# Kernel optimization log

Measured on AMD Instinct MI355X. Metric: run time of the kernel, lower is better.

Reference implementation:

```python
import jax, jax.numpy as jnp
from jax import lax
import numpy as np

NUM_SUBCNNS = 3      # num_classes - 1
C_FEAT = 1024        # backbone feature channels (hard-coded in CAM loop)
STRIDE = 32          # 224 -> 7 spatial reduction, like densenet121 features


def setup_inputs() -> dict:
    key = jax.random.key(0)
    ks = jax.random.split(key, 8)
    B, H, W = 32, 224, 224
    x = jax.random.normal(ks[0], (B, 3, H, W), dtype=jnp.float32)
    # Stand-in backbone per branch: conv 3->1024, kernel=stride=32 (same output
    # shape/dataflow as densenet121 features: [B,1024,7,7]).
    Wb = jax.random.normal(ks[1], (NUM_SUBCNNS, C_FEAT, 3, STRIDE, STRIDE), dtype=jnp.float32) * 0.02
    bb = jnp.zeros((NUM_SUBCNNS, C_FEAT), dtype=jnp.float32)
    # projection head: Linear(1024,512) -> ReLU -> (Dropout, eval=identity) -> Linear(512,2)
    p1_w = jax.random.normal(ks[2], (NUM_SUBCNNS, 512, C_FEAT), dtype=jnp.float32) * 0.02
    p1_b = jnp.zeros((NUM_SUBCNNS, 512), dtype=jnp.float32)
    p2_w = jax.random.normal(ks[3], (NUM_SUBCNNS, 2, 512), dtype=jnp.float32) * 0.02
    p2_b = jnp.zeros((NUM_SUBCNNS, 2), dtype=jnp.float32)
    # classifier Linear(1024,2): only its weight is used, for the CAM reduction
    cls_w = jax.random.normal(ks[4], (NUM_SUBCNNS, 2, C_FEAT), dtype=jnp.float32) * 0.02
    return {"x": x, "Wb": Wb, "bb": bb, "p1_w": p1_w, "p1_b": p1_b,
            "p2_w": p2_w, "p2_b": p2_b, "cls_w": cls_w}


def reference(x, Wb, bb, p1_w, p1_b, p2_w, p2_b, cls_w):
    ranking_outputs = []
    cam_outputs = []
    features_list = []
    for i in range(NUM_SUBCNNS):
        # backbone feature extraction: [B,3,224,224] -> [B,1024,7,7]
        feats = lax.conv_general_dilated(
            x, Wb[i], window_strides=(STRIDE, STRIDE), padding="VALID",
            dimension_numbers=("NCHW", "OIHW", "NCHW")) + bb[i][None, :, None, None]
        features_list.append(feats)
        # global average pool over H,W
        pooled = jnp.mean(feats, axis=(2, 3))                       # [B,1024]
        # projection MLP (dropout is identity at inference)
        h = jax.nn.relu(pooled @ p1_w[i].T + p1_b[i])               # [B,512]
        logits = h @ p2_w[i].T + p2_b[i]                            # [B,2]
        ranking_outputs.append(jax.nn.softmax(logits, axis=1)[:, 1:2])  # [B,1]
        # CAM: the torch double python-loop == one contraction over channels
        cam = jax.nn.relu(jnp.einsum("oc,bchw->obhw", cls_w[i], feats))  # [2,B,7,7]
        cam_outputs.append((cam[0], cam[1]))
    ranking = jnp.concatenate(ranking_outputs, axis=1)              # [B,3]
    return ranking, cam_outputs, features_list
```

## Files before the change

kernel.cpp:

```cpp
#include <hip/hip_runtime.h>
#include <hip/hip_bf16.h>
#include <math.h>

#define NSUB   3
#define CFEAT  1024
#define KDIM   3072
#define MDIM   1568
#define BATCH  32
#define NK     48

#define OUT_CAM   96
#define OUT_FEAT  9504
#define FEAT_PER_BRANCH (BATCH * CFEAT * 49)

#define WS_A      0
#define WS_W      (9600 * 1024)
#define WS_POOLED (WS_W + 18432 * 1024)
#define WS_H      (WS_POOLED + NSUB * BATCH * CFEAT * 4)
#define WS_CAMP   (WS_H + NSUB * BATCH * 512 * 4)

typedef __attribute__((ext_vector_type(8))) short bf16x8;
typedef __attribute__((ext_vector_type(4))) float f32x4;

__device__ __forceinline__ short b16(float f){
    __hip_bfloat16 h = __float2bfloat16(f);
    return *reinterpret_cast<short*>(&h);
}
__device__ __forceinline__ bf16x8 pack8(float4 a, float4 b){
    bf16x8 r;
    r[0]=b16(a.x); r[1]=b16(a.y); r[2]=b16(a.z); r[3]=b16(a.w);
    r[4]=b16(b.x); r[5]=b16(b.y); r[6]=b16(b.z); r[7]=b16(b.w);
    return r;
}

typedef const __attribute__((address_space(1))) void* gas1_t;
typedef __attribute__((address_space(3))) void* las3_t;
__device__ __forceinline__ void gl_lds16(const short* g, char* l){
    __builtin_amdgcn_global_load_lds((gas1_t)g, (las3_t)l, 16, 0, 0);
}

__global__ __launch_bounds__(256) void prep_frag(
    const float* __restrict__ x, const float* __restrict__ w,
    bf16x8* __restrict__ Af, bf16x8* __restrict__ Wf)
{
    int bid = blockIdx.x, t = threadIdx.x;
    if (bid < 4608) {
        int g = bid * 256 + t;
        int chunk = g >> 6, l = g & 63;
        int ni = chunk & 3, KT = (chunk >> 2) % 96, NTg = chunk / 384;
        int n = NTg * 64 + ni * 16 + (l & 15);
        int k = KT * 32 + (l >> 4) * 8;
        const float* src = w + (size_t)n * KDIM + k;
        Wf[(size_t)chunk * 64 + l] = pack8(*(const float4*)src, *(const float4*)(src + 4));
    } else {
        int g = (bid - 4608) * 256 + t;
        int chunk = g >> 6, l = g & 63;
        int mi = chunk & 3, KT = (chunk >> 2) % 96, MT = chunk / 384;
        int m  = MT * 64 + mi * 16 + (l & 15);
        int k0 = KT * 32 + (l >> 4) * 8;
        bf16x8 v;
        if (m < MDIM) {
            int b = m / 49, p = m % 49, ph = p / 7, pw = p % 7;
            int ch = k0 >> 10, r = (k0 >> 5) & 31, s = k0 & 31;
            const float* src = x + (((size_t)(b*3 + ch)*224 + ph*32 + r)*224 + pw*32 + s);
            v = pack8(*(const float4*)src, *(const float4*)(src + 4));
        } else {
            v = (bf16x8){0,0,0,0,0,0,0,0};
        }
        Af[(size_t)chunk * 64 + l] = v;
    }
}

__global__ __launch_bounds__(256, 3) void conv_mfma(
    const bf16x8* __restrict__ Af, const bf16x8* __restrict__ Wf,
    const float* __restrict__ bb, float* __restrict__ out)
{
    __shared__ __align__(16) char lds[32768];

    int bid = (int)blockIdx.x;
    bid = (bid & 7) * 78 + (bid >> 3);
    const int i   = bid / 208;
    const int rem = bid % 208;
    const int nt  = rem / 13, mt = rem % 13;

    const int t = threadIdx.x, wv = t >> 6, l = t & 63;
    const int wr = wv >> 1, wc = wv & 1;
    const int lrow = l & 15, lsl = l >> 4;

    const bf16x8* Ag[4]; int Ad[4];
#pragma unroll
    for (int q = 0; q < 4; ++q) {
        int chunk = (2*mt + (wv >> 1))*384 + (wv & 1)*4 + q;
        Ag[q] = Af + (size_t)chunk * 64 + l;
        Ad[q] = (wv*4 + q) * 1024;
    }

    const int NTg = i*16 + nt;
    const bf16x8* Bp[2][2];
#pragma unroll
    for (int ni = 0; ni < 2; ++ni)
#pragma unroll
        for (int kk = 0; kk < 2; ++kk)
            Bp[ni][kk] = Wf + (size_t)(NTg*384 + kk*4 + wc*2 + ni) * 64 + l;

    f32x4 acc[4][2] = {};
    bf16x8 bgA[2][2], bgB[2][2];

#pragma unroll
    for (int q = 0; q < 4; ++q) gl_lds16((const short*)Ag[q], lds + Ad[q]);
#pragma unroll
    for (int ni = 0; ni < 2; ++ni)
#pragma unroll
        for (int kk = 0; kk < 2; ++kk)
            bgA[ni][kk] = *Bp[ni][kk];

    auto COMPUTE = [&](const char* base, bf16x8 (&BG)[2][2]) {
        bf16x8 af[4][2];
#pragma unroll
        for (int kk = 0; kk < 2; ++kk)
#pragma unroll
            for (int mi = 0; mi < 4; ++mi)
                af[mi][kk] = *(const bf16x8*)(base + ((wr*2 + kk)*4 + mi)*1024 + l*16);
        __builtin_amdgcn_s_setprio(1);
#pragma unroll
        for (int kk = 0; kk < 2; ++kk)
#pragma unroll
            for (int mi = 0; mi < 4; ++mi)
#pragma unroll
                for (int ni = 0; ni < 2; ++ni)
                    acc[mi][ni] = __builtin_amdgcn_mfma_f32_16x16x32_bf16(
                        af[mi][kk], BG[ni][kk], acc[mi][ni], 0, 0, 0);
        __builtin_amdgcn_s_setprio(0);
    };

    for (int kt = 0; kt < NK; kt += 2) {
        __syncthreads();
        if (kt + 1 < NK) {
#pragma unroll
            for (int q = 0; q < 4; ++q)
                gl_lds16((const short*)(Ag[q] + (kt+1)*512), lds + 16384 + Ad[q]);
#pragma unroll
            for (int ni = 0; ni < 2; ++ni)
#pragma unroll
                for (int kk = 0; kk < 2; ++kk)
                    bgB[ni][kk] = Bp[ni][kk][(size_t)(kt+1)*512];
        }
        COMPUTE(lds, bgA);
        __syncthreads();
        if (kt + 2 < NK) {
#pragma unroll
            for (int q = 0; q < 4; ++q)
                gl_lds16((const short*)(Ag[q] + (kt+2)*512), lds + Ad[q]);
#pragma unroll
            for (int ni = 0; ni < 2; ++ni)
#pragma unroll
                for (int kk = 0; kk < 2; ++kk)
                    bgA[ni][kk] = Bp[ni][kk][(size_t)(kt+2)*512];
        }
        COMPUTE(lds + 16384, bgB);
    }

    float* featb = out + OUT_FEAT + (size_t)i * FEAT_PER_BRANCH;
    float bias[2];
#pragma unroll
    for (int ni = 0; ni < 2; ++ni)
        bias[ni] = bb[i*CFEAT + nt*64 + wc*32 + ni*16 + lrow];
#pragma unroll
    for (int mi = 0; mi < 4; ++mi) {
        int mbase = mt*128 + wr*64 + mi*16 + lsl*4;
#pragma unroll
        for (int r = 0; r < 4; ++r) {
            int m = mbase + r;
            if (m >= MDIM) continue;
            int b = m/49, p = m%49;
#pragma unroll
            for (int ni = 0; ni < 2; ++ni) {
                int n = nt*64 + wc*32 + ni*16 + lrow;
                featb[(size_t)(b*CFEAT + n)*49 + p] = acc[mi][ni][r] + bias[ni];
            }
        }
    }
}

__global__ __launch_bounds__(128) void cam_pool(
    const float* __restrict__ feat, const float* __restrict__ cls_w,
    float* __restrict__ pooled, float* __restrict__ camp)
{
    __shared__ float fs[128][50];
    int bid = blockIdx.x;
    int i = bid >> 8, b = (bid >> 3) & 31, ch = bid & 7;
    int t = threadIdx.x;
    int c0 = ch * 128;
    const float* f = feat + ((size_t)(i*BATCH + b) * CFEAT + c0) * 49;

    for (int qq = 0; qq < 49; ++qq) {
        int e = qq*128 + t;
        fs[e / 49][e % 49] = f[e];
    }
    __syncthreads();

    {
        float s = 0.f;
#pragma unroll
        for (int k = 0; k < 49; ++k) s += fs[t][k];
        pooled[(size_t)(i*BATCH + b) * CFEAT + c0 + t] = s * (1.f/49.f);
    }

    if (t < 98) {
        int o = t / 49, p = t % 49;
        const float* w = cls_w + (size_t)i * 2 * CFEAT + o * CFEAT + c0;
        float s = 0.f;
        for (int c = 0; c < 128; ++c) s += w[c] * fs[c][p];
        camp[(size_t)bid * 98 + t] = s;
    }
}

__global__ __launch_bounds__(256) void mlp1_kernel(
    const float* __restrict__ pooled, const float* __restrict__ p1w,
    const float* __restrict__ p1b, float* __restrict__ h,
    const float* __restrict__ camp, float* __restrict__ out_cam)
{
    if (blockIdx.x >= 48) {
        int fid = (blockIdx.x - 48) * 256 + threadIdx.x;
        if (fid < NSUB * 2 * MDIM) {
            int io = fid / MDIM, rem = fid % MDIM;
            int b = rem / 49, p = rem % 49;
            int i = io >> 1, o = io & 1;
            float s = 0.f;
#pragma unroll
            for (int c = 0; c < 8; ++c)
                s += camp[(size_t)(((i*BATCH + b)*8) + c) * 98 + o*49 + p];
            out_cam[fid] = fmaxf(s, 0.f);
        }
        return;
    }
    __shared__ float ps[32 * 256];
    int i = blockIdx.x >> 4, jc = blockIdx.x & 15;
    int t = threadIdx.x;
    int j = jc*32 + (t & 31);
    int bg = (t >> 5) * 4;
    float acc[4] = {};
    const float* wrow = p1w + ((size_t)i*512 + j) * CFEAT;
    for (int kc = 0; kc < 4; ++kc) {
        __syncthreads();
#pragma unroll
        for (int qq = 0; qq < 8; ++qq) {
            int f4 = t + qq*256;
            int b = f4 >> 6, k4 = (f4 & 63) * 4;
            *(float4*)&ps[b*256 + k4] =
                *(const float4*)&pooled[((size_t)i*32 + b)*CFEAT + kc*256 + k4];
        }
        __syncthreads();
        const float* wk = wrow + kc*256;
        for (int k = 0; k < 256; k += 4) {
            float4 w4 = *(const float4*)(wk + k);
#pragma unroll
            for (int qq = 0; qq < 4; ++qq) {
                const float* pr = &ps[(bg + qq)*256 + k];
                acc[qq] += w4.x*pr[0] + w4.y*pr[1] + w4.z*pr[2] + w4.w*pr[3];
            }
        }
    }
    float bias = p1b[i*512 + j];
#pragma unroll
    for (int qq = 0; qq < 4; ++qq)
        h[((size_t)i*32 + bg + qq)*512 + j] = fmaxf(acc[qq] + bias, 0.f);
}

__global__ void mlp2_kernel(const float* __restrict__ h, const float* __restrict__ p2w,
                            const float* __restrict__ p2b, float* __restrict__ out)
{
    __shared__ float part[256];
    int i = blockIdx.x, t = threadIdx.x;
    int b = t & 31, kc = t >> 5;
    const float* hv = h + ((size_t)i*32 + b)*512 + kc*64;
    const float* w0 = p2w + (size_t)i*1024 + kc*64;
    const float* w1 = w0 + 512;
    float s = 0.f;
    for (int k = 0; k < 64; ++k) s += hv[k] * (w1[k] - w0[k]);
    part[t] = s;
    __syncthreads();
    if (t < 32) {
        float d = 0.f;
#pragma unroll
        for (int qq = 0; qq < 8; ++qq) d += part[qq*32 + t];
        d += p2b[i*2 + 1] - p2b[i*2 + 0];
        out[b*NSUB + i] = 1.f / (1.f + expf(-d));
    }
}

extern "C" void kernel_launch(void* const* d_in, const int* in_sizes, int n_in,
                              void* d_out, int out_size, void* d_ws, size_t ws_size,
                              hipStream_t stream)
{
    const float* x    = (const float*)d_in[0];
    const float* Wb   = (const float*)d_in[1];
    const float* bbp  = (const float*)d_in[2];
    const float* p1w  = (const float*)d_in[3];
    const float* p1b  = (const float*)d_in[4];
    const float* p2w  = (const float*)d_in[5];
    const float* p2b  = (const float*)d_in[6];
    const float* clsw = (const float*)d_in[7];
    float* out = (float*)d_out;

    char* ws = (char*)d_ws;
    bf16x8* Af    = (bf16x8*)(ws + WS_A);
    bf16x8* Wf    = (bf16x8*)(ws + WS_W);
    float* pooled = (float*)(ws + WS_POOLED);
    float* hbuf   = (float*)(ws + WS_H);
    float* camp   = (float*)(ws + WS_CAMP);

    prep_frag<<<4608 + 2400, 256, 0, stream>>>(x, Wb, Af, Wf);
    conv_mfma<<<624, 256, 0, stream>>>(Af, Wf, bbp, out);
    cam_pool<<<NSUB*BATCH*8, 128, 0, stream>>>(out + OUT_FEAT, clsw, pooled, camp);
    mlp1_kernel<<<48 + 37, 256, 0, stream>>>(pooled, p1w, p1b, hbuf, camp, out + OUT_CAM);
    mlp2_kernel<<<NSUB, 256, 0, stream>>>(hbuf, p2w, p2b, out);
}
```

Measured before the change: 117.5 us.

## Split conv GEMM K dimension across two wave groups with LDS reduction

Doubles the conv_mfma block to 512 threads and gives each half of the waves half of the K range (24 K-tiles each), using separate LDS double buffers per half. At the end, the second half writes its partial accumulators to LDS and the first half adds them along with the bias before storing features. This targets the long serial K loop per block, since only 624 blocks exist, by putting more waves per tile. The cost is twice the LDS, an extra reduction pass through shared memory, and possibly lower occupancy.

```diff
diff --git a/kernel.cpp b/kernel.cpp
--- a/kernel.cpp
+++ b/kernel.cpp
@@ -7,7 +7,7 @@
 #define KDIM   3072
 #define MDIM   1568
 #define BATCH  32
-#define NK     48
+#define NKL    24
 
 #define OUT_CAM   96
 #define OUT_FEAT  9504
@@ -71,11 +71,11 @@
     }
 }
 
-__global__ __launch_bounds__(256, 3) void conv_mfma(
+__global__ __launch_bounds__(512, 4) void conv_mfma(
     const bf16x8* __restrict__ Af, const bf16x8* __restrict__ Wf,
     const float* __restrict__ bb, float* __restrict__ out)
 {
-    __shared__ __align__(16) char lds[32768];
+    __shared__ __align__(16) char lds[65536];
 
     int bid = (int)blockIdx.x;
     bid = (bid & 7) * 78 + (bid >> 3);
@@ -84,15 +84,19 @@
     const int nt  = rem / 13, mt = rem % 13;
 
     const int t = threadIdx.x, wv = t >> 6, l = t & 63;
-    const int wr = wv >> 1, wc = wv & 1;
+    const int h   = wv >> 2;
+    const int ws2 = wv & 3;
+    const int wr  = ws2 >> 1, wc = ws2 & 1;
     const int lrow = l & 15, lsl = l >> 4;
-
-    const bf16x8* Ag[4]; int Ad[4];
+    const int hbase = h * 32768;
+
+    const short* Ag[4]; int Ad[4];
 #pragma unroll
     for (int q = 0; q < 4; ++q) {
-        int chunk = (2*mt + (wv >> 1))*384 + (wv & 1)*4 + q;
-        Ag[q] = Af + (size_t)chunk * 64 + l;
-        Ad[q] = (wv*4 + q) * 1024;
+        int sl  = ws2*4 + q;
+        int m64 = sl >> 3, kk = (sl >> 2) & 1, mi = sl & 3;
+        Ag[q] = (const short*)(Af + (size_t)((2*mt + m64)*384 + h*192 + kk*4 + mi) * 64 + l);
+        Ad[q] = hbase + sl * 1024;
     }
 
     const int NTg = i*16 + nt;
@@ -101,26 +105,27 @@
     for (int ni = 0; ni < 2; ++ni)
 #pragma unroll
         for (int kk = 0; kk < 2; ++kk)
-            Bp[ni][kk] = Wf + (size_t)(NTg*384 + kk*4 + wc*2 + ni) * 64 + l;
+            Bp[ni][kk] = Wf + (size_t)(NTg*384 + h*192 + kk*4 + wc*2 + ni) * 64 + l;
 
     f32x4 acc[4][2] = {};
     bf16x8 bgA[2][2], bgB[2][2];
 
 #pragma unroll
-    for (int q = 0; q < 4; ++q) gl_lds16((const short*)Ag[q], lds + Ad[q]);
+    for (int q = 0; q < 4; ++q) gl_lds16(Ag[q], lds + Ad[q]);
 #pragma unroll
     for (int ni = 0; ni < 2; ++ni)
 #pragma unroll
         for (int kk = 0; kk < 2; ++kk)
             bgA[ni][kk] = *Bp[ni][kk];
 
-    auto COMPUTE = [&](const char* base, bf16x8 (&BG)[2][2]) {
+    auto COMPUTE = [&](int bufsel, bf16x8 (&BG)[2][2]) {
+        const char* base = lds + hbase + bufsel * 16384;
         bf16x8 af[4][2];
 #pragma unroll
         for (int kk = 0; kk < 2; ++kk)
 #pragma unroll
             for (int mi = 0; mi < 4; ++mi)
-                af[mi][kk] = *(const bf16x8*)(base + ((wr*2 + kk)*4 + mi)*1024 + l*16);
+                af[mi][kk] = *(const bf16x8*)(base + (wr*8 + kk*4 + mi)*1024 + l*16);
         __builtin_amdgcn_s_setprio(1);
 #pragma unroll
         for (int kk = 0; kk < 2; ++kk)
@@ -133,50 +138,67 @@
         __builtin_amdgcn_s_setprio(0);
     };
 
-    for (int kt = 0; kt < NK; kt += 2) {
+    for (int ktl = 0; ktl < NKL; ktl += 2) {
         __syncthreads();
-        if (kt + 1 < NK) {
+        if (ktl + 1 < NKL) {
 #pragma unroll
             for (int q = 0; q < 4; ++q)
-                gl_lds16((const short*)(Ag[q] + (kt+1)*512), lds + 16384 + Ad[q]);
+                gl_lds16(Ag[q] + (size_t)(ktl+1)*512*8, lds + 16384 + Ad[q]);
 #pragma unroll
             for (int ni = 0; ni < 2; ++ni)
 #pragma unroll
                 for (int kk = 0; kk < 2; ++kk)
-                    bgB[ni][kk] = Bp[ni][kk][(size_t)(kt+1)*512];
-        }
-        COMPUTE(lds, bgA);
+                    bgB[ni][kk] = Bp[ni][kk][(size_t)(ktl+1)*512];
+        }
+        COMPUTE(0, bgA);
         __syncthreads();
-        if (kt + 2 < NK) {
+        if (ktl + 2 < NKL) {
 #pragma unroll
             for (int q = 0; q < 4; ++q)
-                gl_lds16((const short*)(Ag[q] + (kt+2)*512), lds + Ad[q]);
+                gl_lds16(Ag[q] + (size_t)(ktl+2)*512*8, lds + Ad[q]);
 #pragma unroll
             for (int ni = 0; ni < 2; ++ni)
 #pragma unroll
                 for (int kk = 0; kk < 2; ++kk)
-                    bgA[ni][kk] = Bp[ni][kk][(size_t)(kt+2)*512];
-        }
-        COMPUTE(lds + 16384, bgB);
-    }
-
-    float* featb = out + OUT_FEAT + (size_t)i * FEAT_PER_BRANCH;
-    float bias[2];
-#pragma unroll
-    for (int ni = 0; ni < 2; ++ni)
-        bias[ni] = bb[i*CFEAT + nt*64 + wc*32 + ni*16 + lrow];
-#pragma unroll
-    for (int mi = 0; mi < 4; ++mi) {
-        int mbase = mt*128 + wr*64 + mi*16 + lsl*4;
-#pragma unroll
-        for (int r = 0; r < 4; ++r) {
-            int m = mbase + r;
-            if (m >= MDIM) continue;
-            int b = m/49, p = m%49;
-#pragma unroll
-            for (int ni = 0; ni < 2; ++ni) {
-                int n = nt*64 + wc*32 + ni*16 + lrow;
-                featb[(size_t)(b*CFEAT + n)*49 + p] = acc[mi][ni][r] + bias[ni];
+                    bgA[ni][kk] = Bp[ni][kk][(size_t)(ktl+2)*512];
+        }
+        COMPUTE(1, bgB);
+    }
+
+    __syncthreads();
+    float* red = (float*)lds;
+    if (h == 1) {
+#pragma unroll
+        for (int mi = 0; mi < 4; ++mi)
+#pragma unroll
+            for (int ni = 0; ni < 2; ++ni)
+#pragma unroll
+                for (int r = 0; r < 4; ++r)
+                    red[ws2*2112 + (mi*16 + lsl*4 + r)*33 + ni*16 + lrow] = acc[mi][ni][r];
+    }
+    __syncthreads();
+    if (h == 0) {
+        float bias[2];
+#pragma unroll
+        for (int ni = 0; ni < 2; ++ni)
+            bias[ni] = bb[i*CFEAT + nt*64 + wc*32 + ni*16 + lrow];
+        float* featb = out + OUT_FEAT + (size_t)i * FEAT_PER_BRANCH;
+#pragma unroll
+        for (int mi = 0; mi < 4; ++mi) {
+            int mbase = mt*128 + wr*64 + mi*16 + lsl*4;
+#pragma unroll
+            for (int r = 0; r < 4; ++r) {
+                int m = mbase + r;
+                if (m >= MDIM) continue;
+                int b = m/49, p = m%49;
+#pragma unroll
+                for (int ni = 0; ni < 2; ++ni) {
+                    int n = nt*64 + wc*32 + ni*16 + lrow;
+                    float v = acc[mi][ni][r]
+                            + red[ws2*2112 + (mi*16 + lsl*4 + r)*33 + ni*16 + lrow]
+                            + bias[ni];
+                    featb[(size_t)(b*CFEAT + n)*49 + p] = v;
+                }
             }
         }
     }
@@ -311,7 +333,7 @@
     float* camp   = (float*)(ws + WS_CAMP);
 
     prep_frag<<<4608 + 2400, 256, 0, stream>>>(x, Wb, Af, Wf);
-    conv_mfma<<<624, 256, 0, stream>>>(Af, Wf, bbp, out);
+    conv_mfma<<<624, 512, 0, stream>>>(Af, Wf, bbp, out);
     cam_pool<<<NSUB*BATCH*8, 128, 0, stream>>>(out + OUT_FEAT, clsw, pooled, camp);
     mlp1_kernel<<<48 + 37, 256, 0, stream>>>(pooled, p1w, p1b, hbuf, camp, out + OUT_CAM);
     mlp2_kernel<<<NSUB, 256, 0, stream>>>(hbuf, p2w, p2b, out);
```

Result: slower. 121.9 us (+3.7%).
